# Performance work log

Hardware: AMD Instinct MI355X
Metric: run time of the kernel (lower is better)

## Reference

```python
import jax, jax.numpy as jnp
import numpy as np

B, S, D, DFF = 4, 2048, 1024, 4096
EPS = 1e-5


def layernorm(x, g, b):
    mu = jnp.mean(x, axis=-1, keepdims=True)
    var = jnp.mean(jnp.square(x - mu), axis=-1, keepdims=True)
    return (x - mu) * jax.lax.rsqrt(var + EPS) * g + b


def setup_inputs() -> dict:
    key = jax.random.key(0)
    ks = jax.random.split(key, 4)
    hidden_state = jax.random.normal(ks[0], (B, S, D), dtype=jnp.float32)
    attention_mask = jnp.zeros((B, 1, S), dtype=jnp.float32)  # additive mask
    w1 = jax.random.normal(ks[1], (D, DFF), dtype=jnp.float32) * (1.0 / np.sqrt(D))
    b1 = jnp.zeros((DFF,), dtype=jnp.float32)
    w2 = jax.random.normal(ks[2], (DFF, D), dtype=jnp.float32) * (1.0 / np.sqrt(DFF))
    b2 = jnp.zeros((D,), dtype=jnp.float32)
    ln1_g = jnp.ones((D,), dtype=jnp.float32)
    ln1_b = jnp.zeros((D,), dtype=jnp.float32)
    ln2_g = jnp.ones((D,), dtype=jnp.float32)
    ln2_b = jnp.zeros((D,), dtype=jnp.float32)
    return dict(hidden_state=hidden_state, attention_mask=attention_mask,
                w1=w1, b1=b1, w2=w2, b2=b2,
                ln1_g=ln1_g, ln1_b=ln1_b, ln2_g=ln2_g, ln2_b=ln2_b)


def reference(hidden_state, attention_mask, w1, b1, w2, b2, ln1_g, ln1_b, ln2_g, ln2_b):
    x = hidden_state
    d = jnp.asarray(x.shape[-1], x.dtype)
    # hand-rolled single-head attention: q=k=v=x (source forward ignores QKV projections)
    scores = jnp.einsum('bqd,bkd->bqk', x, x) / jnp.sqrt(d) + attention_mask  # [B,S,S]
    attn = jax.nn.softmax(scores, axis=-1)
    attn_out = jnp.einsum('bqk,bkd->bqd', attn, x)
    h = layernorm(x + attn_out, ln1_g, ln1_b)
    # FFN: dense -> exact GELU -> linear_2
    ffn = jnp.einsum('bsf,fd->bsd', jax.nn.gelu(jnp.einsum('bsd,df->bsf', h, w1) + b1, approximate=False), w2) + b2
    return layernorm(h + ffn, ln2_g, ln2_b)
```

## Files before the change

### kernel.cpp

```cpp
#include <hip/hip_runtime.h>
#include <hip/hip_bf16.h>
#include <math.h>

#define LN_EPS 1e-5f

typedef short short8 __attribute__((ext_vector_type(8)));
typedef float floatx4 __attribute__((ext_vector_type(4)));

__device__ inline unsigned short f2bf(float f) {
    unsigned int u = __float_as_uint(f);
    u += 0x7fff + ((u >> 16) & 1);
    return (unsigned short)(u >> 16);
}

__device__ inline void gl_lds16(const unsigned short* g, unsigned short* l) {
    __builtin_amdgcn_global_load_lds(
        (__attribute__((address_space(1))) const void*)g,
        (__attribute__((address_space(3))) void*)l, 16, 0, 0);
}

__device__ inline float gelu_f(float v) {
    float u2 = 2.0f * v * (0.7978845608f + 0.0356774081f * v * v);
    float t  = 1.0f - 2.0f / (__expf(u2) + 1.0f);
    return 0.5f * v * (1.0f + t);
}

#define CFENCE asm volatile("" ::: "memory")

template<int EPI, int BN>
__global__ __launch_bounds__(512, 2) void gemm8p(
    const unsigned short* __restrict__ A, const unsigned short* __restrict__ B,
    const float* __restrict__ bias, const float* __restrict__ resid,
    void* __restrict__ Cptr,
    int M, int N, int K, long sA, long sB, long sC, long sBias, float scale)
{
    static_assert(BN == 256 || BN == 128, "BN must be 256 or 128");
    constexpr int WC = BN / 4;
    constexpr int NT = WC / 16;
    constexpr int NH = NT / 2;

    __shared__ alignas(16) unsigned short lds_a[2][2][256 * 32];
    __shared__ alignas(16) unsigned short lds_b[2][2][BN * 32];

    const int tid  = threadIdx.x;
    const int lane = tid & 63;
    const int wave = tid >> 6;
    const int quad = lane >> 4;
    const int l16  = lane & 15;
    const int wm = wave >> 2;
    const int wn = wave & 3;

    const int nwg = gridDim.x * gridDim.y * gridDim.z;
    int lin = blockIdx.x + gridDim.x * (blockIdx.y + gridDim.y * blockIdx.z);
    if ((nwg & 7) == 0) lin = (lin & 7) * (nwg >> 3) + (lin >> 3);
    const int bx = lin % gridDim.x;
    const int byz = lin / gridDim.x;
    const int by = byz % gridDim.y;
    const int bz = byz / gridDim.y;

    const int tile_m = by * 256;
    const int tile_n = bx * BN;
    const int batch  = bz;

    const unsigned short* Ab = A + (size_t)batch * sA;
    const unsigned short* Bb = B + (size_t)batch * sB;

    const int srow = tid >> 2;
    const int scs  = ((tid & 3) ^ ((tid & 32) ? 2 : 0)) * 8;
    const unsigned short* gA = Ab + (size_t)(tile_m + srow) * K + scs;
    const unsigned short* gB = Bb + (size_t)(tile_n + srow) * K + scs;
    const int ldst = tid * 8;

    const int kcs   = (quad * 8) ^ ((l16 & 8) << 1);
    const int abase = (wm * 128 + l16) * 32 + kcs;
    const int bbase = (wn * WC  + l16) * 32 + kcs;

    floatx4 acc[8][NT];
    const floatx4 zero = {0.f, 0.f, 0.f, 0.f};
#pragma unroll
    for (int i = 0; i < 8; i++)
#pragma unroll
        for (int j = 0; j < NT; j++) acc[i][j] = zero;

    auto stageA = [&](int buf, int h, int k0) {
        const unsigned short* s = gA + (size_t)h * 128 * K + k0;
        gl_lds16(s,      &lds_a[buf][0][h * 4096 + ldst]);
        gl_lds16(s + 32, &lds_a[buf][1][h * 4096 + ldst]);
    };
    auto stageB = [&](int buf, int h, int k0) {
        const unsigned short* s = gB + (size_t)h * 128 * K + k0;
        gl_lds16(s,      &lds_b[buf][0][h * 4096 + ldst]);
        gl_lds16(s + 32, &lds_b[buf][1][h * 4096 + ldst]);
    };

    const int nt = K >> 6;

    stageA(0, 0, 0); stageA(0, 1, 0);
    stageB(0, 0, 0);
    if constexpr (BN == 256) stageB(0, 1, 0);
    if (nt > 1) {
        stageB(1, 0, 64);
        if constexpr (BN == 256) stageB(1, 1, 64);
        if constexpr (BN == 256) { asm volatile("s_waitcnt vmcnt(4)" ::: "memory"); }
        else                     { asm volatile("s_waitcnt vmcnt(2)" ::: "memory"); }
    } else {
        asm volatile("s_waitcnt vmcnt(0)" ::: "memory");
    }
    __builtin_amdgcn_s_barrier(); CFENCE;

    int cur = 0;
    for (int t = 0; t < nt; ++t) {
        const int k0 = t * 64;
        short8 afr[4][2], bfrA[NH][2], bfrB[NH][2];

#pragma unroll
        for (int i = 0; i < 4; i++)
#pragma unroll
            for (int kh = 0; kh < 2; kh++)
                afr[i][kh] = *(const short8*)&lds_a[cur][kh][abase + i * 512];
#pragma unroll
        for (int j = 0; j < NH; j++)
#pragma unroll
            for (int kh = 0; kh < 2; kh++)
                bfrA[j][kh] = *(const short8*)&lds_b[cur][kh][bbase + j * 512];
        if (t + 1 < nt) stageA(cur ^ 1, 0, k0 + 64);
        CFENCE; __builtin_amdgcn_s_barrier(); CFENCE;
        __builtin_amdgcn_s_setprio(1);
#pragma unroll
        for (int i = 0; i < 4; i++)
#pragma unroll
            for (int j = 0; j < NH; j++)
#pragma unroll
                for (int kh = 0; kh < 2; kh++)
                    acc[i][j] = __builtin_amdgcn_mfma_f32_16x16x32_bf16(
                        bfrA[j][kh], afr[i][kh], acc[i][j], 0, 0, 0);
        __builtin_amdgcn_s_setprio(0);
        CFENCE; __builtin_amdgcn_s_barrier(); CFENCE;

#pragma unroll
        for (int j = 0; j < NH; j++)
#pragma unroll
            for (int kh = 0; kh < 2; kh++)
                bfrB[j][kh] = *(const short8*)&lds_b[cur][kh][bbase + (NH + j) * 512];
        if (t + 1 < nt) stageA(cur ^ 1, 1, k0 + 64);
        CFENCE; __builtin_amdgcn_s_barrier(); CFENCE;
        __builtin_amdgcn_s_setprio(1);
#pragma unroll
        for (int i = 0; i < 4; i++)
#pragma unroll
            for (int j = 0; j < NH; j++)
#pragma unroll
                for (int kh = 0; kh < 2; kh++)
                    acc[i][NH + j] = __builtin_amdgcn_mfma_f32_16x16x32_bf16(
                        bfrB[j][kh], afr[i][kh], acc[i][NH + j], 0, 0, 0);
        __builtin_amdgcn_s_setprio(0);
        CFENCE; __builtin_amdgcn_s_barrier(); CFENCE;

#pragma unroll
        for (int i = 0; i < 4; i++)
#pragma unroll
            for (int kh = 0; kh < 2; kh++)
                afr[i][kh] = *(const short8*)&lds_a[cur][kh][abase + (4 + i) * 512];
        if (t + 2 < nt) stageB(cur, 0, k0 + 128);
        CFENCE; __builtin_amdgcn_s_barrier(); CFENCE;
        __builtin_amdgcn_s_setprio(1);
#pragma unroll
        for (int i = 0; i < 4; i++)
#pragma unroll
            for (int j = 0; j < NH; j++)
#pragma unroll
                for (int kh = 0; kh < 2; kh++)
                    acc[4 + i][NH + j] = __builtin_amdgcn_mfma_f32_16x16x32_bf16(
                        bfrB[j][kh], afr[i][kh], acc[4 + i][NH + j], 0, 0, 0);
        __builtin_amdgcn_s_setprio(0);
        CFENCE; __builtin_amdgcn_s_barrier(); CFENCE;

        if constexpr (BN == 256) { if (t + 2 < nt) stageB(cur, 1, k0 + 128); }
        __builtin_amdgcn_s_setprio(1);
#pragma unroll
        for (int i = 0; i < 4; i++)
#pragma unroll
            for (int j = 0; j < NH; j++)
#pragma unroll
                for (int kh = 0; kh < 2; kh++)
                    acc[4 + i][j] = __builtin_amdgcn_mfma_f32_16x16x32_bf16(
                        bfrA[j][kh], afr[i][kh], acc[4 + i][j], 0, 0, 0);
        __builtin_amdgcn_s_setprio(0);
        if (t + 3 <= nt) {
            if constexpr (BN == 256) { asm volatile("s_waitcnt vmcnt(4)" ::: "memory"); }
            else                     { asm volatile("s_waitcnt vmcnt(2)" ::: "memory"); }
            __builtin_amdgcn_s_barrier(); CFENCE;
        } else if (t + 2 == nt) {
            asm volatile("s_waitcnt vmcnt(0)" ::: "memory");
            __builtin_amdgcn_s_barrier(); CFENCE;
        }
        cur ^= 1;
    }

#pragma unroll
    for (int i = 0; i < 8; i++) {
        const int row = tile_m + wm * 128 + i * 16 + l16;
#pragma unroll
        for (int j = 0; j < NT; j++) {
            const int colb = tile_n + wn * WC + j * 16 + quad * 4;
            float v[4];
#pragma unroll
            for (int r = 0; r < 4; r++) v[r] = acc[i][j][r];

            if (EPI == 3) {
                float4 mv = *(const float4*)&bias[(size_t)batch * sBias + colb];
                v[0] = v[0] * scale + mv.x;  v[1] = v[1] * scale + mv.y;
                v[2] = v[2] * scale + mv.z;  v[3] = v[3] * scale + mv.w;
            }
            if (EPI == 2 || EPI == 5) {
                float4 bv = *(const float4*)&bias[colb];
                v[0] += bv.x; v[1] += bv.y; v[2] += bv.z; v[3] += bv.w;
            }
            if (EPI == 2) {
#pragma unroll
                for (int r = 0; r < 4; r++) v[r] = gelu_f(v[r]);
            }
            if (EPI == 4 || EPI == 5) {
                float4 rv = *(const float4*)&resid[(size_t)batch * sC +
                                                   (size_t)row * N + colb];
                v[0] += rv.x; v[1] += rv.y; v[2] += rv.z; v[3] += rv.w;
            }

            if (EPI == 2 || EPI == 3) {
                unsigned short* C = (unsigned short*)Cptr + (size_t)batch * sC;
                ushort4 h4;
                h4.x = f2bf(v[0]); h4.y = f2bf(v[1]);
                h4.z = f2bf(v[2]); h4.w = f2bf(v[3]);
                *(ushort4*)(C + (size_t)row * N + colb) = h4;
            } else {
                float* C = (float*)Cptr + (size_t)batch * sC;
                float4 f4 = {v[0], v[1], v[2], v[3]};
                *(float4*)(C + (size_t)row * N + colb) = f4;
            }
        }
    }
}

__global__ __launch_bounds__(256) void x_prep_kernel(
    const float* __restrict__ in, unsigned short* __restrict__ straight,
    unsigned short* __restrict__ transposed, int R, int C, long sIn)
{
    __shared__ float tile[32][33];
    const int tc = blockIdx.x * 32, tr = blockIdx.y * 32;
    const float* src = in + (size_t)blockIdx.z * sIn;
    unsigned short* dstS = straight   + (size_t)blockIdx.z * sIn;
    unsigned short* dstT = transposed + (size_t)blockIdx.z * sIn;
    const int tx = threadIdx.x & 31, ty = threadIdx.x >> 5;
#pragma unroll
    for (int i = 0; i < 4; i++) {
        float val = src[(size_t)(tr + ty + i * 8) * C + tc + tx];
        tile[ty + i * 8][tx] = val;
        dstS[(size_t)(tr + ty + i * 8) * C + tc + tx] = f2bf(val);
    }
    __syncthreads();
#pragma unroll
    for (int i = 0; i < 4; i++)
        dstT[(size_t)(tc + ty + i * 8) * R + tr + tx] = f2bf(tile[tx][ty + i * 8]);
}

__global__ __launch_bounds__(256) void transpose_cvt_kernel(
    const float* __restrict__ in, unsigned short* __restrict__ out, int R, int C)
{
    __shared__ float tile[32][33];
    const int tc = blockIdx.x * 32, tr = blockIdx.y * 32;
    const int tx = threadIdx.x & 31, ty = threadIdx.x >> 5;
#pragma unroll
    for (int i = 0; i < 4; i++)
        tile[ty + i * 8][tx] = in[(size_t)(tr + ty + i * 8) * C + tc + tx];
    __syncthreads();
#pragma unroll
    for (int i = 0; i < 4; i++)
        out[(size_t)(tc + ty + i * 8) * R + tr + tx] = f2bf(tile[tx][ty + i * 8]);
}

__global__ __launch_bounds__(256) void softmax_bf16_kernel(
    const unsigned short* __restrict__ scores, unsigned short* __restrict__ probs,
    int S)
{
    __shared__ float red[4];
    const int row = blockIdx.x;
    const unsigned short* p = scores + (size_t)row * S;
    unsigned short* pr      = probs  + (size_t)row * S;
    const int tid  = threadIdx.x;
    const int lane = tid & 63;
    const int wav  = tid >> 6;

    uint4 raw = *(const uint4*)(p + tid * 8);
    float v[8];
    v[0] = __uint_as_float(raw.x << 16); v[1] = __uint_as_float(raw.x & 0xffff0000u);
    v[2] = __uint_as_float(raw.y << 16); v[3] = __uint_as_float(raw.y & 0xffff0000u);
    v[4] = __uint_as_float(raw.z << 16); v[5] = __uint_as_float(raw.z & 0xffff0000u);
    v[6] = __uint_as_float(raw.w << 16); v[7] = __uint_as_float(raw.w & 0xffff0000u);

    float mx = v[0];
#pragma unroll
    for (int k = 1; k < 8; k++) mx = fmaxf(mx, v[k]);
#pragma unroll
    for (int off = 32; off > 0; off >>= 1) mx = fmaxf(mx, __shfl_down(mx, off));
    if (lane == 0) red[wav] = mx;
    __syncthreads();
    mx = fmaxf(fmaxf(red[0], red[1]), fmaxf(red[2], red[3]));
    __syncthreads();

    float s = 0.f;
#pragma unroll
    for (int k = 0; k < 8; k++) { v[k] = __expf(v[k] - mx); s += v[k]; }
#pragma unroll
    for (int off = 32; off > 0; off >>= 1) s += __shfl_down(s, off);
    if (lane == 0) red[wav] = s;
    __syncthreads();
    s = red[0] + red[1] + red[2] + red[3];
    float inv = 1.0f / s;

    uint4 o;
    o.x = (unsigned)f2bf(v[0] * inv) | ((unsigned)f2bf(v[1] * inv) << 16);
    o.y = (unsigned)f2bf(v[2] * inv) | ((unsigned)f2bf(v[3] * inv) << 16);
    o.z = (unsigned)f2bf(v[4] * inv) | ((unsigned)f2bf(v[5] * inv) << 16);
    o.w = (unsigned)f2bf(v[6] * inv) | ((unsigned)f2bf(v[7] * inv) << 16);
    *(uint4*)(pr + tid * 8) = o;
}

template<int WRITE_BF16>
__global__ __launch_bounds__(256) void ln_kernel(
    const float* __restrict__ X,
    const float* __restrict__ g, const float* __restrict__ bta,
    float* __restrict__ out, unsigned short* __restrict__ out16, int D)
{
    __shared__ float red[8];
    const int row = blockIdx.x;
    const float* x = X + (size_t)row * D;
    const int tid  = threadIdx.x;
    const int lane = tid & 63;
    const int wav  = tid >> 6;

    float4 a = *(const float4*)(x + tid * 4);
    float v0 = a.x, v1 = a.y, v2 = a.z, v3 = a.w;

    float s1 = v0 + v1 + v2 + v3;
    float s2 = v0 * v0 + v1 * v1 + v2 * v2 + v3 * v3;
#pragma unroll
    for (int off = 32; off > 0; off >>= 1) {
        s1 += __shfl_down(s1, off);
        s2 += __shfl_down(s2, off);
    }
    if (lane == 0) { red[wav] = s1; red[4 + wav] = s2; }
    __syncthreads();
    s1 = red[0] + red[1] + red[2] + red[3];
    s2 = red[4] + red[5] + red[6] + red[7];
    const float mu  = s1 / (float)D;
    const float var = s2 / (float)D - mu * mu;
    const float rs  = rsqrtf(var + LN_EPS);

    float4 gg = *(const float4*)(g + tid * 4);
    float4 bb = *(const float4*)(bta + tid * 4);
    float4 r;
    r.x = (v0 - mu) * rs * gg.x + bb.x;
    r.y = (v1 - mu) * rs * gg.y + bb.y;
    r.z = (v2 - mu) * rs * gg.z + bb.z;
    r.w = (v3 - mu) * rs * gg.w + bb.w;
    *(float4*)(out + (size_t)row * D + tid * 4) = r;
    if (WRITE_BF16) {
        ushort4 h;
        h.x = f2bf(r.x); h.y = f2bf(r.y); h.z = f2bf(r.z); h.w = f2bf(r.w);
        *(ushort4*)(out16 + (size_t)row * D + tid * 4) = h;
    }
}

extern "C" void kernel_launch(void* const* d_in, const int* in_sizes, int n_in,
                              void* d_out, int out_size, void* d_ws, size_t ws_size,
                              hipStream_t stream) {
    (void)in_sizes; (void)n_in; (void)out_size; (void)ws_size;
    const float* x    = (const float*)d_in[0];
    const float* mask = (const float*)d_in[1];
    const float* w1   = (const float*)d_in[2];
    const float* b1   = (const float*)d_in[3];
    const float* w2   = (const float*)d_in[4];
    const float* b2   = (const float*)d_in[5];
    const float* ln1g = (const float*)d_in[6];
    const float* ln1b = (const float*)d_in[7];
    const float* ln2g = (const float*)d_in[8];
    const float* ln2b = (const float*)d_in[9];
    float* out = (float*)d_out;

    const int B = 4, S = 2048, D = 1024, DFF = 4096;
    const size_t MB = 1024 * 1024;

    char* ws = (char*)d_ws;
    unsigned short* scoresb = (unsigned short*)ws;
    unsigned short* act     = (unsigned short*)ws;
    unsigned short* xb      = (unsigned short*)(ws + 32 * MB);
    unsigned short* probs   = (unsigned short*)(ws + 32 * MB);
    float*          hbuf    = (float*)(ws + 64 * MB);
    unsigned short* hb16    = (unsigned short*)(ws + 96 * MB);
    unsigned short* w1T     = (unsigned short*)(ws + 112 * MB);
    unsigned short* w2T     = (unsigned short*)(ws + 120 * MB);
    unsigned short* xTb     = (unsigned short*)d_out;
    float*          fsum    = (float*)d_out;

    x_prep_kernel<<<dim3(D / 32, S / 32, B), 256, 0, stream>>>(
        x, xb, xTb, S, D, (long)S * D);
    transpose_cvt_kernel<<<dim3(DFF / 32, D / 32, 1), 256, 0, stream>>>(w1, w1T, D, DFF);
    transpose_cvt_kernel<<<dim3(D / 32, DFF / 32, 1), 256, 0, stream>>>(w2, w2T, DFF, D);

    hipLaunchKernelGGL((gemm8p<3, 256>), dim3(S / 256, S / 256, B), dim3(512), 0, stream,
                       xb, xb, mask, (const float*)nullptr, (void*)scoresb,
                       S, S, D, (long)S * D, (long)S * D, (long)S * S, (long)S, 0.03125f);
    softmax_bf16_kernel<<<B * S, 256, 0, stream>>>(scoresb, probs, S);
    hipLaunchKernelGGL((gemm8p<4, 128>), dim3(D / 128, S / 256, B), dim3(512), 0, stream,
                       probs, xTb, (const float*)nullptr, x, (void*)hbuf,
                       S, D, S, (long)S * S, (long)D * S, (long)S * D, 0L, 0.f);
    hipLaunchKernelGGL((ln_kernel<1>), dim3(B * S), dim3(256), 0, stream,
                       hbuf, ln1g, ln1b, hbuf, hb16, D);
    hipLaunchKernelGGL((gemm8p<2, 256>), dim3(DFF / 256, (B * S) / 256, 1), dim3(512), 0, stream,
                       hb16, w1T, b1, (const float*)nullptr, (void*)act,
                       B * S, DFF, D, 0L, 0L, 0L, 0L, 0.f);
    hipLaunchKernelGGL((gemm8p<5, 128>), dim3(D / 128, (B * S) / 256, 1), dim3(512), 0, stream,
                       act, w2T, b2, hbuf, (void*)fsum,
                       B * S, D, DFF, 0L, 0L, 0L, 0L, 0.f);
    hipLaunchKernelGGL((ln_kernel<0>), dim3(B * S), dim3(256), 0, stream,
                       fsum, ln2g, ln2b, out, (unsigned short*)nullptr, D);
}
```

Baseline: 430.7 us.

## Use split-K with 256-wide tiles for N=1024 GEMMs, reducing in LayerNorm

The two GEMMs with N=1024 (attention-weighted sum and FFN down-projection) move from 128-wide N tiles to 256-wide tiles and split K in half. Each half writes its partial sum to a separate fp32 buffer, and the following LayerNorm kernel adds the two partials. This keeps the grid size similar while raising arithmetic intensity per tile. In exchange it writes and reads an extra fp32 partial buffer, and the MFMA loop order is reordered to put kh outermost.

```diff
diff --git a/kernel.cpp b/kernel.cpp
--- a/kernel.cpp
+++ b/kernel.cpp
@@ -27,20 +27,16 @@
 
 #define CFENCE asm volatile("" ::: "memory")
 
-template<int EPI, int BN>
+template<int EPI>
 __global__ __launch_bounds__(512, 2) void gemm8p(
     const unsigned short* __restrict__ A, const unsigned short* __restrict__ B,
     const float* __restrict__ bias, const float* __restrict__ resid,
-    void* __restrict__ Cptr,
-    int M, int N, int K, long sA, long sB, long sC, long sBias, float scale)
+    void* __restrict__ Cptr, float* __restrict__ C2,
+    int M, int N, int K, long ldA, long ldB,
+    long sA, long sB, long sC, long sBias, int zmod, float scale)
 {
-    static_assert(BN == 256 || BN == 128, "BN must be 256 or 128");
-    constexpr int WC = BN / 4;
-    constexpr int NT = WC / 16;
-    constexpr int NH = NT / 2;
-
     __shared__ alignas(16) unsigned short lds_a[2][2][256 * 32];
-    __shared__ alignas(16) unsigned short lds_b[2][2][BN * 32];
+    __shared__ alignas(16) unsigned short lds_b[2][2][256 * 32];
 
     const int tid  = threadIdx.x;
     const int lane = tid & 63;
@@ -59,36 +55,38 @@
     const int bz = byz / gridDim.y;
 
     const int tile_m = by * 256;
-    const int tile_n = bx * BN;
-    const int batch  = bz;
-
-    const unsigned short* Ab = A + (size_t)batch * sA;
-    const unsigned short* Bb = B + (size_t)batch * sB;
+    const int tile_n = bx * 256;
+    const int batch  = bz % zmod;
+    const int ks     = bz / zmod;
+    const size_t koff = (size_t)ks * K;
+
+    const unsigned short* Ab = A + (size_t)batch * sA + koff;
+    const unsigned short* Bb = B + (size_t)batch * sB + koff;
 
     const int srow = tid >> 2;
     const int scs  = ((tid & 3) ^ ((tid & 32) ? 2 : 0)) * 8;
-    const unsigned short* gA = Ab + (size_t)(tile_m + srow) * K + scs;
-    const unsigned short* gB = Bb + (size_t)(tile_n + srow) * K + scs;
+    const unsigned short* gA = Ab + (size_t)(tile_m + srow) * ldA + scs;
+    const unsigned short* gB = Bb + (size_t)(tile_n + srow) * ldB + scs;
     const int ldst = tid * 8;
 
     const int kcs   = (quad * 8) ^ ((l16 & 8) << 1);
     const int abase = (wm * 128 + l16) * 32 + kcs;
-    const int bbase = (wn * WC  + l16) * 32 + kcs;
-
-    floatx4 acc[8][NT];
+    const int bbase = (wn * 64  + l16) * 32 + kcs;
+
+    floatx4 acc[8][4];
     const floatx4 zero = {0.f, 0.f, 0.f, 0.f};
 #pragma unroll
     for (int i = 0; i < 8; i++)
 #pragma unroll
-        for (int j = 0; j < NT; j++) acc[i][j] = zero;
+        for (int j = 0; j < 4; j++) acc[i][j] = zero;
 
     auto stageA = [&](int buf, int h, int k0) {
-        const unsigned short* s = gA + (size_t)h * 128 * K + k0;
+        const unsigned short* s = gA + (size_t)h * 128 * ldA + k0;
         gl_lds16(s,      &lds_a[buf][0][h * 4096 + ldst]);
         gl_lds16(s + 32, &lds_a[buf][1][h * 4096 + ldst]);
     };
     auto stageB = [&](int buf, int h, int k0) {
-        const unsigned short* s = gB + (size_t)h * 128 * K + k0;
+        const unsigned short* s = gB + (size_t)h * 128 * ldB + k0;
         gl_lds16(s,      &lds_b[buf][0][h * 4096 + ldst]);
         gl_lds16(s + 32, &lds_b[buf][1][h * 4096 + ldst]);
     };
@@ -96,13 +94,10 @@
     const int nt = K >> 6;
 
     stageA(0, 0, 0); stageA(0, 1, 0);
-    stageB(0, 0, 0);
-    if constexpr (BN == 256) stageB(0, 1, 0);
+    stageB(0, 0, 0); stageB(0, 1, 0);
     if (nt > 1) {
-        stageB(1, 0, 64);
-        if constexpr (BN == 256) stageB(1, 1, 64);
-        if constexpr (BN == 256) { asm volatile("s_waitcnt vmcnt(4)" ::: "memory"); }
-        else                     { asm volatile("s_waitcnt vmcnt(2)" ::: "memory"); }
+        stageB(1, 0, 64); stageB(1, 1, 64);
+        asm volatile("s_waitcnt vmcnt(4)" ::: "memory");
     } else {
         asm volatile("s_waitcnt vmcnt(0)" ::: "memory");
     }
@@ -111,7 +106,7 @@
     int cur = 0;
     for (int t = 0; t < nt; ++t) {
         const int k0 = t * 64;
-        short8 afr[4][2], bfrA[NH][2], bfrB[NH][2];
+        short8 afr[4][2], bfrA[2][2], bfrB[2][2];
 
 #pragma unroll
         for (int i = 0; i < 4; i++)
@@ -119,7 +114,7 @@
             for (int kh = 0; kh < 2; kh++)
                 afr[i][kh] = *(const short8*)&lds_a[cur][kh][abase + i * 512];
 #pragma unroll
-        for (int j = 0; j < NH; j++)
+        for (int j = 0; j < 2; j++)
 #pragma unroll
             for (int kh = 0; kh < 2; kh++)
                 bfrA[j][kh] = *(const short8*)&lds_b[cur][kh][bbase + j * 512];
@@ -127,32 +122,32 @@
         CFENCE; __builtin_amdgcn_s_barrier(); CFENCE;
         __builtin_amdgcn_s_setprio(1);
 #pragma unroll
-        for (int i = 0; i < 4; i++)
-#pragma unroll
-            for (int j = 0; j < NH; j++)
-#pragma unroll
-                for (int kh = 0; kh < 2; kh++)
+        for (int kh = 0; kh < 2; kh++)
+#pragma unroll
+            for (int i = 0; i < 4; i++)
+#pragma unroll
+                for (int j = 0; j < 2; j++)
                     acc[i][j] = __builtin_amdgcn_mfma_f32_16x16x32_bf16(
                         bfrA[j][kh], afr[i][kh], acc[i][j], 0, 0, 0);
         __builtin_amdgcn_s_setprio(0);
         CFENCE; __builtin_amdgcn_s_barrier(); CFENCE;
 
 #pragma unroll
-        for (int j = 0; j < NH; j++)
+        for (int j = 0; j < 2; j++)
 #pragma unroll
             for (int kh = 0; kh < 2; kh++)
-                bfrB[j][kh] = *(const short8*)&lds_b[cur][kh][bbase + (NH + j) * 512];
+                bfrB[j][kh] = *(const short8*)&lds_b[cur][kh][bbase + (2 + j) * 512];
         if (t + 1 < nt) stageA(cur ^ 1, 1, k0 + 64);
         CFENCE; __builtin_amdgcn_s_barrier(); CFENCE;
         __builtin_amdgcn_s_setprio(1);
 #pragma unroll
-        for (int i = 0; i < 4; i++)
-#pragma unroll
-            for (int j = 0; j < NH; j++)
-#pragma unroll
-                for (int kh = 0; kh < 2; kh++)
-                    acc[i][NH + j] = __builtin_amdgcn_mfma_f32_16x16x32_bf16(
-                        bfrB[j][kh], afr[i][kh], acc[i][NH + j], 0, 0, 0);
+        for (int kh = 0; kh < 2; kh++)
+#pragma unroll
+            for (int i = 0; i < 4; i++)
+#pragma unroll
+                for (int j = 0; j < 2; j++)
+                    acc[i][2 + j] = __builtin_amdgcn_mfma_f32_16x16x32_bf16(
+                        bfrB[j][kh], afr[i][kh], acc[i][2 + j], 0, 0, 0);
         __builtin_amdgcn_s_setprio(0);
         CFENCE; __builtin_amdgcn_s_barrier(); CFENCE;
 
@@ -165,30 +160,29 @@
         CFENCE; __builtin_amdgcn_s_barrier(); CFENCE;
         __builtin_amdgcn_s_setprio(1);
 #pragma unroll
-        for (int i = 0; i < 4; i++)
-#pragma unroll
-            for (int j = 0; j < NH; j++)
-#pragma unroll
-                for (int kh = 0; kh < 2; kh++)
-                    acc[4 + i][NH + j] = __builtin_amdgcn_mfma_f32_16x16x32_bf16(
-                        bfrB[j][kh], afr[i][kh], acc[4 + i][NH + j], 0, 0, 0);
+        for (int kh = 0; kh < 2; kh++)
+#pragma unroll
+            for (int i = 0; i < 4; i++)
+#pragma unroll
+                for (int j = 0; j < 2; j++)
+                    acc[4 + i][2 + j] = __builtin_amdgcn_mfma_f32_16x16x32_bf16(
+                        bfrB[j][kh], afr[i][kh], acc[4 + i][2 + j], 0, 0, 0);
         __builtin_amdgcn_s_setprio(0);
         CFENCE; __builtin_amdgcn_s_barrier(); CFENCE;
 
-        if constexpr (BN == 256) { if (t + 2 < nt) stageB(cur, 1, k0 + 128); }
+        if (t + 2 < nt) stageB(cur, 1, k0 + 128);
         __builtin_amdgcn_s_setprio(1);
 #pragma unroll
-        for (int i = 0; i < 4; i++)
-#pragma unroll
-            for (int j = 0; j < NH; j++)
-#pragma unroll
-                for (int kh = 0; kh < 2; kh++)
+        for (int kh = 0; kh < 2; kh++)
+#pragma unroll
+            for (int i = 0; i < 4; i++)
+#pragma unroll
+                for (int j = 0; j < 2; j++)
                     acc[4 + i][j] = __builtin_amdgcn_mfma_f32_16x16x32_bf16(
                         bfrA[j][kh], afr[i][kh], acc[4 + i][j], 0, 0, 0);
         __builtin_amdgcn_s_setprio(0);
         if (t + 3 <= nt) {
-            if constexpr (BN == 256) { asm volatile("s_waitcnt vmcnt(4)" ::: "memory"); }
-            else                     { asm volatile("s_waitcnt vmcnt(2)" ::: "memory"); }
+            asm volatile("s_waitcnt vmcnt(4)" ::: "memory");
             __builtin_amdgcn_s_barrier(); CFENCE;
         } else if (t + 2 == nt) {
             asm volatile("s_waitcnt vmcnt(0)" ::: "memory");
@@ -201,8 +195,8 @@
     for (int i = 0; i < 8; i++) {
         const int row = tile_m + wm * 128 + i * 16 + l16;
 #pragma unroll
-        for (int j = 0; j < NT; j++) {
-            const int colb = tile_n + wn * WC + j * 16 + quad * 4;
+        for (int j = 0; j < 4; j++) {
+            const int colb = tile_n + wn * 64 + j * 16 + quad * 4;
             float v[4];
 #pragma unroll
             for (int r = 0; r < 4; r++) v[r] = acc[i][j][r];
@@ -212,15 +206,17 @@
                 v[0] = v[0] * scale + mv.x;  v[1] = v[1] * scale + mv.y;
                 v[2] = v[2] * scale + mv.z;  v[3] = v[3] * scale + mv.w;
             }
-            if (EPI == 2 || EPI == 5) {
+            if (EPI == 2) {
                 float4 bv = *(const float4*)&bias[colb];
                 v[0] += bv.x; v[1] += bv.y; v[2] += bv.z; v[3] += bv.w;
-            }
-            if (EPI == 2) {
 #pragma unroll
                 for (int r = 0; r < 4; r++) v[r] = gelu_f(v[r]);
             }
-            if (EPI == 4 || EPI == 5) {
+            if ((EPI == 4 || EPI == 5) && ks == 0) {
+                if (EPI == 5) {
+                    float4 bv = *(const float4*)&bias[colb];
+                    v[0] += bv.x; v[1] += bv.y; v[2] += bv.z; v[3] += bv.w;
+                }
                 float4 rv = *(const float4*)&resid[(size_t)batch * sC +
                                                    (size_t)row * N + colb];
                 v[0] += rv.x; v[1] += rv.y; v[2] += rv.z; v[3] += rv.w;
@@ -233,7 +229,7 @@
                 h4.z = f2bf(v[2]); h4.w = f2bf(v[3]);
                 *(ushort4*)(C + (size_t)row * N + colb) = h4;
             } else {
-                float* C = (float*)Cptr + (size_t)batch * sC;
+                float* C = (ks ? C2 : (float*)Cptr) + (size_t)batch * sC;
                 float4 f4 = {v[0], v[1], v[2], v[3]};
                 *(float4*)(C + (size_t)row * N + colb) = f4;
             }
@@ -325,9 +321,9 @@
     *(uint4*)(pr + tid * 8) = o;
 }
 
-template<int WRITE_BF16>
+template<int WRITE_BF16, int ADD2>
 __global__ __launch_bounds__(256) void ln_kernel(
-    const float* __restrict__ X,
+    const float* __restrict__ X, const float* __restrict__ X2,
     const float* __restrict__ g, const float* __restrict__ bta,
     float* __restrict__ out, unsigned short* __restrict__ out16, int D)
 {
@@ -340,6 +336,10 @@
 
     float4 a = *(const float4*)(x + tid * 4);
     float v0 = a.x, v1 = a.y, v2 = a.z, v3 = a.w;
+    if (ADD2) {
+        float4 a2 = *(const float4*)(X2 + (size_t)row * D + tid * 4);
+        v0 += a2.x; v1 += a2.y; v2 += a2.z; v3 += a2.w;
+    }
 
     float s1 = v0 + v1 + v2 + v3;
     float s2 = v0 * v0 + v1 * v1 + v2 * v2 + v3 * v3;
@@ -399,6 +399,8 @@
     unsigned short* hb16    = (unsigned short*)(ws + 96 * MB);
     unsigned short* w1T     = (unsigned short*)(ws + 112 * MB);
     unsigned short* w2T     = (unsigned short*)(ws + 120 * MB);
+    float*          hbuf2   = (float*)(ws + 128 * MB);
+    float*          fsum2   = (float*)(ws + 160 * MB);
     unsigned short* xTb     = (unsigned short*)d_out;
     float*          fsum    = (float*)d_out;
 
@@ -407,21 +409,25 @@
     transpose_cvt_kernel<<<dim3(DFF / 32, D / 32, 1), 256, 0, stream>>>(w1, w1T, D, DFF);
     transpose_cvt_kernel<<<dim3(D / 32, DFF / 32, 1), 256, 0, stream>>>(w2, w2T, DFF, D);
 
-    hipLaunchKernelGGL((gemm8p<3, 256>), dim3(S / 256, S / 256, B), dim3(512), 0, stream,
+    hipLaunchKernelGGL((gemm8p<3>), dim3(S / 256, S / 256, B), dim3(512), 0, stream,
                        xb, xb, mask, (const float*)nullptr, (void*)scoresb,
-                       S, S, D, (long)S * D, (long)S * D, (long)S * S, (long)S, 0.03125f);
+                       (float*)nullptr, S, S, D, (long)D, (long)D,
+                       (long)S * D, (long)S * D, (long)S * S, (long)S, B, 0.03125f);
     softmax_bf16_kernel<<<B * S, 256, 0, stream>>>(scoresb, probs, S);
-    hipLaunchKernelGGL((gemm8p<4, 128>), dim3(D / 128, S / 256, B), dim3(512), 0, stream,
-                       probs, xTb, (const float*)nullptr, x, (void*)hbuf,
-                       S, D, S, (long)S * S, (long)D * S, (long)S * D, 0L, 0.f);
-    hipLaunchKernelGGL((ln_kernel<1>), dim3(B * S), dim3(256), 0, stream,
-                       hbuf, ln1g, ln1b, hbuf, hb16, D);
-    hipLaunchKernelGGL((gemm8p<2, 256>), dim3(DFF / 256, (B * S) / 256, 1), dim3(512), 0, stream,
+    hipLaunchKernelGGL((gemm8p<4>), dim3(D / 256, S / 256, B * 2), dim3(512), 0, stream,
+                       probs, xTb, (const float*)nullptr, x, (void*)hbuf, hbuf2,
+                       S, D, S / 2, (long)S, (long)S,
+                       (long)S * S, (long)D * S, (long)S * D, 0L, B, 0.f);
+    hipLaunchKernelGGL((ln_kernel<1, 1>), dim3(B * S), dim3(256), 0, stream,
+                       hbuf, hbuf2, ln1g, ln1b, hbuf, hb16, D);
+    hipLaunchKernelGGL((gemm8p<2>), dim3(DFF / 256, (B * S) / 256, 1), dim3(512), 0, stream,
                        hb16, w1T, b1, (const float*)nullptr, (void*)act,
-                       B * S, DFF, D, 0L, 0L, 0L, 0L, 0.f);
-    hipLaunchKernelGGL((gemm8p<5, 128>), dim3(D / 128, (B * S) / 256, 1), dim3(512), 0, stream,
-                       act, w2T, b2, hbuf, (void*)fsum,
-                       B * S, D, DFF, 0L, 0L, 0L, 0L, 0.f);
-    hipLaunchKernelGGL((ln_kernel<0>), dim3(B * S), dim3(256), 0, stream,
-                       fsum, ln2g, ln2b, out, (unsigned short*)nullptr, D);
-}
+                       (float*)nullptr, B * S, DFF, D, (long)D, (long)D,
+                       0L, 0L, 0L, 0L, 1, 0.f);
+    hipLaunchKernelGGL((gemm8p<5>), dim3(D / 256, (B * S) / 256, 2), dim3(512), 0, stream,
+                       act, w2T, b2, hbuf, (void*)fsum, fsum2,
+                       B * S, D, DFF / 2, (long)DFF, (long)DFF,
+                       0L, 0L, 0L, 0L, 1, 0.f);
+    hipLaunchKernelGGL((ln_kernel<0, 1>), dim3(B * S), dim3(256), 0, stream,
+                       fsum, fsum2, ln2g, ln2b, out, (unsigned short*)nullptr, D);
+}
```

Result: no change. 426.2 us (-1.1%).
